# Kernel optimization log

Hardware: AMD Instinct MI355X
Metric: run time of the kernel (lower is better)

## Reference

```python
import jax, jax.numpy as jnp
import numpy as np

B_SZ, SEQ, D_MODEL = 64, 2048, 12
D_INNER, D_STATE, D_CONV, DT_RANK = 24, 16, 4, 4


def setup_inputs() -> dict:
    key = jax.random.key(0)
    ks = jax.random.split(key, 10)
    def n(k, shape, scale):
        return jax.random.normal(k, shape, jnp.float32) * scale
    return {
        "x": jax.random.normal(ks[0], (B_SZ, SEQ, D_MODEL), jnp.float32),
        "in_proj_w": n(ks[1], (2 * D_INNER, D_MODEL), 0.2),
        "conv_w": n(ks[2], (D_INNER, 1, D_CONV), 0.3),
        "conv_b": jnp.zeros((D_INNER,), jnp.float32),
        "x_proj_w": n(ks[3], (DT_RANK + 2 * D_STATE, D_INNER), 0.2),
        "dt_proj_w": n(ks[4], (D_INNER, DT_RANK), 0.5),
        "dt_proj_b": jax.random.uniform(ks[5], (D_INNER,), jnp.float32, -4.0, -2.0),
        "A_log": jnp.log(jnp.broadcast_to(jnp.arange(1, D_STATE + 1, dtype=jnp.float32), (D_INNER, D_STATE))),
        "D": jnp.ones((D_INNER,), jnp.float32),
        "out_proj_w": n(ks[6], (D_MODEL, D_INNER), 0.2),
        "fc_w": n(ks[7], (1, D_MODEL), 0.3),
        "fc_b": jnp.zeros((1,), jnp.float32),
    }


def _silu(v):
    return v * jax.nn.sigmoid(v)


def _mamba_head(x, in_proj_w, conv_w, conv_b, x_proj_w, dt_proj_w, dt_proj_b,
                A_log, D, out_proj_w, fc_w, fc_b):
    di = A_log.shape[0]
    ds = A_log.shape[1]
    dtr = dt_proj_w.shape[1]
    dc = conv_w.shape[-1]
    bsz = x.shape[0]

    # input projection -> [B,L,2*di], split into ssm branch and gate
    xz = jnp.einsum('bld,ed->ble', x, in_proj_w)
    x_in, z = jnp.split(xz, 2, axis=-1)

    # causal depthwise conv1d over time
    x_t = jnp.transpose(x_in, (0, 2, 1))                       # [B,di,L]
    x_t = jnp.pad(x_t, ((0, 0), (0, 0), (dc - 1, 0)))
    xc = jax.lax.conv_general_dilated(x_t, conv_w, (1,), 'VALID',
                                      feature_group_count=di)
    xc = _silu(jnp.transpose(xc + conv_b[None, :, None], (0, 2, 1)))  # [B,L,di]

    # data-dependent dt, B, C
    x_dbl = jnp.einsum('bld,ed->ble', xc, x_proj_w)
    dt, Bm, Cm = jnp.split(x_dbl, [dtr, dtr + ds], axis=-1)
    dt = jax.nn.softplus(jnp.einsum('blr,dr->bld', dt, dt_proj_w) + dt_proj_b)  # [B,L,di]

    A = -jnp.exp(A_log)                                        # [di,ds]
    dA = jnp.exp(dt[..., None] * A)                            # [B,L,di,ds]
    dBu = dt[..., None] * Bm[:, :, None, :] * xc[..., None]    # [B,L,di,ds]

    def step(h, inp):
        dA_t, dBu_t, C_t = inp
        h = dA_t * h + dBu_t                                   # [B,di,ds]
        y = jnp.einsum('bds,bs->bd', h, C_t)
        return h, y

    h0 = jnp.zeros((bsz, di, ds), x.dtype)
    _, ys = jax.lax.scan(step, h0, (jnp.swapaxes(dA, 0, 1),
                                    jnp.swapaxes(dBu, 0, 1),
                                    jnp.swapaxes(Cm, 0, 1)))
    y = jnp.swapaxes(ys, 0, 1) + xc * D                        # [B,L,di]
    y = y * _silu(z)
    out = jnp.einsum('bld,ed->ble', y, out_proj_w)             # [B,L,d_model]

    # final head on last timestep (SimpleMamba.linear)
    pred = out[:, -1, :] @ fc_w.T + fc_b                       # [B,1]
    return pred


def reference(x, in_proj_w, conv_w, conv_b, x_proj_w, dt_proj_w, dt_proj_b,
              A_log, D, out_proj_w, fc_w, fc_b):
    return _mamba_head(x, in_proj_w, conv_w, conv_b, x_proj_w, dt_proj_w,
                       dt_proj_b, A_log, D, out_proj_w, fc_w, fc_b)
```

## Files before the change

### kernel.cpp

```cpp
#include <hip/hip_runtime.h>
#include <math.h>

#define B_SZ 64
#define SEQ 2048
#define DM 12
#define DI 24
#define DS 16
#define DC 4
#define DTR 4
#define NSEG 32
#define SEGLEN 64
#define LP 68

__device__ __forceinline__ float silu_f(float v) { return v / (1.f + __expf(-v)); }
__device__ __forceinline__ float softplus_f(float v) {
    return fmaxf(v, 0.f) + __logf(1.f + __expf(-fabsf(v)));
}
__device__ __forceinline__ float dot12(const float4 w[3], float4 r0, float4 r1, float4 r2) {
    float s = 0.f;
    s = fmaf(w[0].x, r0.x, s); s = fmaf(w[0].y, r0.y, s);
    s = fmaf(w[0].z, r0.z, s); s = fmaf(w[0].w, r0.w, s);
    s = fmaf(w[1].x, r1.x, s); s = fmaf(w[1].y, r1.y, s);
    s = fmaf(w[1].z, r1.z, s); s = fmaf(w[1].w, r1.w, s);
    s = fmaf(w[2].x, r2.x, s); s = fmaf(w[2].y, r2.y, s);
    s = fmaf(w[2].z, r2.z, s); s = fmaf(w[2].w, r2.w, s);
    return s;
}

__global__ __launch_bounds__(384) void fused_scan_kernel(
    const float* __restrict__ x, const float* __restrict__ ipw,
    const float* __restrict__ cw, const float* __restrict__ cb,
    const float* __restrict__ xpw, const float* __restrict__ dpw,
    const float* __restrict__ dpb, const float* __restrict__ A_log,
    float* __restrict__ segA, float* __restrict__ segB)
{
    __shared__ __align__(16) float xc_s[DI][LP];
    __shared__ __align__(16) float dts[DI][LP];
    __shared__ __align__(16) float Bs[DS][LP];
    __shared__ __align__(16) float dtr_s[DTR][LP];

    const int tid = threadIdx.x;
    const int b = blockIdx.x >> 5, seg = blockIdx.x & 31;
    const int t0 = seg * SEGLEN;
    const int j = tid >> 6;
    const int t = tid & 63;
    const int d0 = j * 4;

    const float Aval = -__expf(A_log[tid]);

    float xc_loc[4];
    {
        float4 wA[4][3];
        float cwr[4][4];
        float acc[4];
#pragma unroll
        for (int i = 0; i < 4; ++i) {
            const float4* wp = (const float4*)(ipw + (d0 + i) * DM);
            wA[i][0] = wp[0]; wA[i][1] = wp[1]; wA[i][2] = wp[2];
            const float4 cw4 = *(const float4*)(cw + (d0 + i) * DC);
            cwr[i][0] = cw4.x; cwr[i][1] = cw4.y; cwr[i][2] = cw4.z; cwr[i][3] = cw4.w;
            acc[i] = cb[d0 + i];
        }
#pragma unroll
        for (int k = 0; k < DC; ++k) {
            int gt = t0 + t - (DC - 1) + k;
            float4 r0, r1, r2;
            if (gt >= 0) {
                const float4* xp = (const float4*)(x + ((size_t)b * SEQ + gt) * DM);
                r0 = xp[0]; r1 = xp[1]; r2 = xp[2];
            } else {
                r0 = make_float4(0.f, 0.f, 0.f, 0.f); r1 = r0; r2 = r0;
            }
#pragma unroll
            for (int i = 0; i < 4; ++i) {
                float xin = dot12(wA[i], r0, r1, r2);
                acc[i] = fmaf(xin, cwr[i][k], acc[i]);
            }
        }
#pragma unroll
        for (int i = 0; i < 4; ++i) {
            float v = silu_f(acc[i]);
            xc_loc[i] = v;
            xc_s[d0 + i][t] = v;
        }
    }
    __syncthreads();

    {
        float xc[DI];
#pragma unroll
        for (int d = 0; d < DI; ++d) xc[d] = xc_s[d][t];
        for (int r = j; r < DTR + DS; r += 6) {
            const float4* wr = (const float4*)(xpw + r * DI);
            float4 w4[6];
#pragma unroll
            for (int c = 0; c < 6; ++c) w4[c] = wr[c];
            float s = 0.f;
#pragma unroll
            for (int c = 0; c < 6; ++c) {
                s = fmaf(w4[c].x, xc[4 * c + 0], s);
                s = fmaf(w4[c].y, xc[4 * c + 1], s);
                s = fmaf(w4[c].z, xc[4 * c + 2], s);
                s = fmaf(w4[c].w, xc[4 * c + 3], s);
            }
            if (r < DTR) dtr_s[r][t] = s;
            else         Bs[r - DTR][t] = s;
        }
    }
    __syncthreads();

    {
        float dtr[DTR];
#pragma unroll
        for (int r = 0; r < DTR; ++r) dtr[r] = dtr_s[r][t];
#pragma unroll
        for (int i = 0; i < 4; ++i) {
            int d = d0 + i;
            const float4 w4 = *(const float4*)(dpw + d * DTR);
            float s = dpb[d];
            s = fmaf(dtr[0], w4.x, s); s = fmaf(dtr[1], w4.y, s);
            s = fmaf(dtr[2], w4.z, s); s = fmaf(dtr[3], w4.w, s);
            float dt = softplus_f(s);
            dts[d][t] = dt;
            xc_s[d][t] = dt * xc_loc[i];
        }
    }
    __syncthreads();

    {
        const int d = tid >> 4, s = tid & 15;
        float a_acc = 1.f, b_acc = 0.f;
        const float4* dtp = (const float4*)&dts[d][0];
        const float4* dup = (const float4*)&xc_s[d][0];
        const float4* Bp  = (const float4*)&Bs[s][0];
#pragma unroll 4
        for (int i = 0; i < SEGLEN / 4; ++i) {
            float4 dt4 = dtp[i], du4 = dup[i], B4 = Bp[i];
            float a;
            a = __expf(dt4.x * Aval); b_acc = fmaf(a, b_acc, du4.x * B4.x); a_acc *= a;
            a = __expf(dt4.y * Aval); b_acc = fmaf(a, b_acc, du4.y * B4.y); a_acc *= a;
            a = __expf(dt4.z * Aval); b_acc = fmaf(a, b_acc, du4.z * B4.z); a_acc *= a;
            a = __expf(dt4.w * Aval); b_acc = fmaf(a, b_acc, du4.w * B4.w); a_acc *= a;
        }
        size_t o = (size_t)blockIdx.x * (DI * DS) + tid;
        segA[o] = a_acc;
        segB[o] = b_acc;
    }
}

__global__ __launch_bounds__(384) void finish_kernel(
    const float* __restrict__ segA, const float* __restrict__ segB,
    const float* __restrict__ x, const float* __restrict__ ipw,
    const float* __restrict__ cw, const float* __restrict__ cb,
    const float* __restrict__ xpw, const float* __restrict__ Dv,
    const float* __restrict__ opw, const float* __restrict__ fcw,
    const float* __restrict__ fcb, float* __restrict__ out)
{
    int b = blockIdx.x, tid = threadIdx.x;

    float h = 0.f;
#pragma unroll
    for (int g = 0; g < NSEG; ++g) {
        size_t o = ((size_t)(b * NSEG + g)) * (DI * DS) + tid;
        h = fmaf(segA[o], h, segB[o]);
    }

    __shared__ float h_sh[DI * DS];
    __shared__ float xcl[DI], CL[DS], zv[DI], yv[DI], ov[DM];
    h_sh[tid] = h;

    const float* xr = x + ((size_t)b * SEQ + SEQ - 1) * DM;
    if (tid < DI) {
        float acc = cb[tid];
#pragma unroll
        for (int k = 0; k < DC; ++k) {
            const float* row = x + ((size_t)b * SEQ + (SEQ - DC + k)) * DM;
            float xin = 0.f;
#pragma unroll
            for (int m = 0; m < DM; ++m) xin = fmaf(row[m], ipw[tid * DM + m], xin);
            acc = fmaf(xin, cw[tid * DC + k], acc);
        }
        xcl[tid] = silu_f(acc);
        float s = 0.f;
#pragma unroll
        for (int m = 0; m < DM; ++m) s = fmaf(xr[m], ipw[(DI + tid) * DM + m], s);
        zv[tid] = s;
    }
    __syncthreads();

    if (tid < DS) {
        float s = 0.f;
#pragma unroll
        for (int d = 0; d < DI; ++d) s = fmaf(xcl[d], xpw[(DTR + DS + tid) * DI + d], s);
        CL[tid] = s;
    }
    __syncthreads();

    if (tid < DI) {
        float y = 0.f;
#pragma unroll
        for (int s2 = 0; s2 < DS; ++s2) y = fmaf(h_sh[tid * DS + s2], CL[s2], y);
        y = fmaf(xcl[tid], Dv[tid], y);
        yv[tid] = y * silu_f(zv[tid]);
    }
    __syncthreads();

    if (tid < DM) {
        float s = 0.f;
#pragma unroll
        for (int d = 0; d < DI; ++d) s = fmaf(yv[d], opw[tid * DI + d], s);
        ov[tid] = s;
    }
    __syncthreads();

    if (tid == 0) {
        float s = fcb[0];
#pragma unroll
        for (int e = 0; e < DM; ++e) s = fmaf(ov[e], fcw[e], s);
        out[b] = s;
    }
}

extern "C" void kernel_launch(void* const* d_in, const int* in_sizes, int n_in,
                              void* d_out, int out_size, void* d_ws, size_t ws_size,
                              hipStream_t stream)
{
    const float* x   = (const float*)d_in[0];
    const float* ipw = (const float*)d_in[1];
    const float* cw  = (const float*)d_in[2];
    const float* cb  = (const float*)d_in[3];
    const float* xpw = (const float*)d_in[4];
    const float* dpw = (const float*)d_in[5];
    const float* dpb = (const float*)d_in[6];
    const float* Al  = (const float*)d_in[7];
    const float* Dv  = (const float*)d_in[8];
    const float* opw = (const float*)d_in[9];
    const float* fcw = (const float*)d_in[10];
    const float* fcb = (const float*)d_in[11];

    float* segA = (float*)d_ws;
    float* segB = segA + (size_t)B_SZ * NSEG * DI * DS;

    fused_scan_kernel<<<B_SZ * NSEG, 384, 0, stream>>>(
        x, ipw, cw, cb, xpw, dpw, dpb, Al, segA, segB);
    finish_kernel<<<B_SZ, 384, 0, stream>>>(
        segA, segB, x, ipw, cw, cb, xpw, Dv, opw, fcw, fcb, (float*)d_out);
}
```

Measured before the change: 117.2 us.

## Fuse finish into scan kernel via last-block atomic counter; stage in_proj in LDS

```diff
diff --git a/kernel.cpp b/kernel.cpp
--- a/kernel.cpp
+++ b/kernel.cpp
@@ -27,17 +27,22 @@
     return s;
 }
 
-__global__ __launch_bounds__(384) void fused_scan_kernel(
+__global__ __launch_bounds__(384) void mamba_one_kernel(
     const float* __restrict__ x, const float* __restrict__ ipw,
     const float* __restrict__ cw, const float* __restrict__ cb,
     const float* __restrict__ xpw, const float* __restrict__ dpw,
     const float* __restrict__ dpb, const float* __restrict__ A_log,
-    float* __restrict__ segA, float* __restrict__ segB)
+    const float* __restrict__ Dv, const float* __restrict__ opw,
+    const float* __restrict__ fcw, const float* __restrict__ fcb,
+    float* __restrict__ segA, float* __restrict__ segB,
+    int* __restrict__ cnt, float* __restrict__ out)
 {
+    __shared__ __align__(16) float xin_s[DI][LP];
     __shared__ __align__(16) float xc_s[DI][LP];
     __shared__ __align__(16) float dts[DI][LP];
     __shared__ __align__(16) float Bs[DS][LP];
     __shared__ __align__(16) float dtr_s[DTR][LP];
+    __shared__ int is_last;
 
     const int tid = threadIdx.x;
     const int b = blockIdx.x >> 5, seg = blockIdx.x & 31;
@@ -48,38 +53,45 @@
 
     const float Aval = -__expf(A_log[tid]);
 
-    float xc_loc[4];
-    {
-        float4 wA[4][3];
-        float cwr[4][4];
-        float acc[4];
+    float4 wA[4][3];
+    float cwr[4][4], cbr[4];
+    {
 #pragma unroll
         for (int i = 0; i < 4; ++i) {
             const float4* wp = (const float4*)(ipw + (d0 + i) * DM);
             wA[i][0] = wp[0]; wA[i][1] = wp[1]; wA[i][2] = wp[2];
             const float4 cw4 = *(const float4*)(cw + (d0 + i) * DC);
             cwr[i][0] = cw4.x; cwr[i][1] = cw4.y; cwr[i][2] = cw4.z; cwr[i][3] = cw4.w;
-            acc[i] = cb[d0 + i];
-        }
-#pragma unroll
-        for (int k = 0; k < DC; ++k) {
-            int gt = t0 + t - (DC - 1) + k;
-            float4 r0, r1, r2;
+            cbr[i] = cb[d0 + i];
+        }
+        const float4* xp = (const float4*)(x + ((size_t)b * SEQ + (t0 + t)) * DM);
+        float4 r0 = xp[0], r1 = xp[1], r2 = xp[2];
+#pragma unroll
+        for (int i = 0; i < 4; ++i) xin_s[d0 + i][t + 3] = dot12(wA[i], r0, r1, r2);
+        if (t < 3) {
+            int gt = t0 + t - 3;
+            float4 h0, h1, h2;
             if (gt >= 0) {
-                const float4* xp = (const float4*)(x + ((size_t)b * SEQ + gt) * DM);
-                r0 = xp[0]; r1 = xp[1]; r2 = xp[2];
+                const float4* hp = (const float4*)(x + ((size_t)b * SEQ + gt) * DM);
+                h0 = hp[0]; h1 = hp[1]; h2 = hp[2];
             } else {
-                r0 = make_float4(0.f, 0.f, 0.f, 0.f); r1 = r0; r2 = r0;
+                h0 = make_float4(0.f, 0.f, 0.f, 0.f); h1 = h0; h2 = h0;
             }
 #pragma unroll
-            for (int i = 0; i < 4; ++i) {
-                float xin = dot12(wA[i], r0, r1, r2);
-                acc[i] = fmaf(xin, cwr[i][k], acc[i]);
-            }
-        }
+            for (int i = 0; i < 4; ++i) xin_s[d0 + i][t] = dot12(wA[i], h0, h1, h2);
+        }
+    }
+    __syncthreads();
+
+    float xc_loc[4];
+    {
 #pragma unroll
         for (int i = 0; i < 4; ++i) {
-            float v = silu_f(acc[i]);
+            float acc = cbr[i];
+#pragma unroll
+            for (int k = 0; k < DC; ++k)
+                acc = fmaf(cwr[i][k], xin_s[d0 + i][t + k], acc);
+            float v = silu_f(acc);
             xc_loc[i] = v;
             xc_s[d0 + i][t] = v;
         }
@@ -122,7 +134,7 @@
             s = fmaf(dtr[2], w4.z, s); s = fmaf(dtr[3], w4.w, s);
             float dt = softplus_f(s);
             dts[d][t] = dt;
-            xc_s[d][t] = dt * xc_loc[i];
+            xin_s[d][t] = dt * xc_loc[i];
         }
     }
     __syncthreads();
@@ -131,7 +143,7 @@
         const int d = tid >> 4, s = tid & 15;
         float a_acc = 1.f, b_acc = 0.f;
         const float4* dtp = (const float4*)&dts[d][0];
-        const float4* dup = (const float4*)&xc_s[d][0];
+        const float4* dup = (const float4*)&xin_s[d][0];
         const float4* Bp  = (const float4*)&Bs[s][0];
 #pragma unroll 4
         for (int i = 0; i < SEGLEN / 4; ++i) {
@@ -146,17 +158,19 @@
         segA[o] = a_acc;
         segB[o] = b_acc;
     }
-}
-
-__global__ __launch_bounds__(384) void finish_kernel(
-    const float* __restrict__ segA, const float* __restrict__ segB,
-    const float* __restrict__ x, const float* __restrict__ ipw,
-    const float* __restrict__ cw, const float* __restrict__ cb,
-    const float* __restrict__ xpw, const float* __restrict__ Dv,
-    const float* __restrict__ opw, const float* __restrict__ fcw,
-    const float* __restrict__ fcb, float* __restrict__ out)
-{
-    int b = blockIdx.x, tid = threadIdx.x;
+    __syncthreads();
+
+    if (tid == 0) {
+        __threadfence();
+        int old = atomicAdd(&cnt[b], 1);
+        is_last = (old == NSEG - 1);
+        if (is_last) __threadfence();
+    }
+    __syncthreads();
+    if (!is_last) return;
+
+    __shared__ float h_sh[DI * DS];
+    __shared__ float xcl[DI], CL[DS], zv[DI], yv[DI], ov[DM];
 
     float h = 0.f;
 #pragma unroll
@@ -164,9 +178,6 @@
         size_t o = ((size_t)(b * NSEG + g)) * (DI * DS) + tid;
         h = fmaf(segA[o], h, segB[o]);
     }
-
-    __shared__ float h_sh[DI * DS];
-    __shared__ float xcl[DI], CL[DS], zv[DI], yv[DI], ov[DM];
     h_sh[tid] = h;
 
     const float* xr = x + ((size_t)b * SEQ + SEQ - 1) * DM;
@@ -240,9 +251,10 @@
 
     float* segA = (float*)d_ws;
     float* segB = segA + (size_t)B_SZ * NSEG * DI * DS;
-
-    fused_scan_kernel<<<B_SZ * NSEG, 384, 0, stream>>>(
-        x, ipw, cw, cb, xpw, dpw, dpb, Al, segA, segB);
-    finish_kernel<<<B_SZ, 384, 0, stream>>>(
-        segA, segB, x, ipw, cw, cb, xpw, Dv, opw, fcw, fcb, (float*)d_out);
-}
+    int*   cnt  = (int*)(segB + (size_t)B_SZ * NSEG * DI * DS);
+
+    hipMemsetAsync(cnt, 0, B_SZ * sizeof(int), stream);
+    mamba_one_kernel<<<B_SZ * NSEG, 384, 0, stream>>>(
+        x, ipw, cw, cb, xpw, dpw, dpb, Al, Dv, opw, fcw, fcb,
+        segA, segB, cnt, (float*)d_out);
+}
```

Measured after the change: 159.2 us. +35.8%, slower.

## Restructure segment scan kernel into single-wave blocks with multi-chain per-thread scans

Applied to the files above, without the earlier changes.

```diff
diff --git a/kernel.cpp b/kernel.cpp
--- a/kernel.cpp
+++ b/kernel.cpp
@@ -16,135 +16,133 @@
 __device__ __forceinline__ float softplus_f(float v) {
     return fmaxf(v, 0.f) + __logf(1.f + __expf(-fabsf(v)));
 }
-__device__ __forceinline__ float dot12(const float4 w[3], float4 r0, float4 r1, float4 r2) {
+__device__ __forceinline__ float dot12w(float4 w0, float4 w1, float4 w2,
+                                        float4 r0, float4 r1, float4 r2) {
     float s = 0.f;
-    s = fmaf(w[0].x, r0.x, s); s = fmaf(w[0].y, r0.y, s);
-    s = fmaf(w[0].z, r0.z, s); s = fmaf(w[0].w, r0.w, s);
-    s = fmaf(w[1].x, r1.x, s); s = fmaf(w[1].y, r1.y, s);
-    s = fmaf(w[1].z, r1.z, s); s = fmaf(w[1].w, r1.w, s);
-    s = fmaf(w[2].x, r2.x, s); s = fmaf(w[2].y, r2.y, s);
-    s = fmaf(w[2].z, r2.z, s); s = fmaf(w[2].w, r2.w, s);
+    s = fmaf(w0.x, r0.x, s); s = fmaf(w0.y, r0.y, s);
+    s = fmaf(w0.z, r0.z, s); s = fmaf(w0.w, r0.w, s);
+    s = fmaf(w1.x, r1.x, s); s = fmaf(w1.y, r1.y, s);
+    s = fmaf(w1.z, r1.z, s); s = fmaf(w1.w, r1.w, s);
+    s = fmaf(w2.x, r2.x, s); s = fmaf(w2.y, r2.y, s);
+    s = fmaf(w2.z, r2.z, s); s = fmaf(w2.w, r2.w, s);
     return s;
 }
 
-__global__ __launch_bounds__(384) void fused_scan_kernel(
+__global__ __launch_bounds__(64) void fused_wave_kernel(
     const float* __restrict__ x, const float* __restrict__ ipw,
     const float* __restrict__ cw, const float* __restrict__ cb,
     const float* __restrict__ xpw, const float* __restrict__ dpw,
     const float* __restrict__ dpb, const float* __restrict__ A_log,
     float* __restrict__ segA, float* __restrict__ segB)
 {
-    __shared__ __align__(16) float xc_s[DI][LP];
-    __shared__ __align__(16) float dts[DI][LP];
-    __shared__ __align__(16) float Bs[DS][LP];
-    __shared__ __align__(16) float dtr_s[DTR][LP];
-
-    const int tid = threadIdx.x;
+    __shared__ __align__(16) float dts_s[DI][LP];
+    __shared__ __align__(16) float dus_s[DI][LP];
+    __shared__ __align__(16) float Bs_s[DS][LP];
+
+    const int lane = threadIdx.x;
     const int b = blockIdx.x >> 5, seg = blockIdx.x & 31;
     const int t0 = seg * SEGLEN;
-    const int j = tid >> 6;
-    const int t = tid & 63;
-    const int d0 = j * 4;
-
-    const float Aval = -__expf(A_log[tid]);
-
-    float xc_loc[4];
+    const int t = lane;
+
+#pragma unroll
+    for (int rep = 0; rep < 2; ++rep) {
+        int pp = lane + rep * 64;
+        if (pp < 3 * DI) {
+            int hr = pp / DI, d = pp % DI;
+            int row = t0 - 3 + hr;
+            float v = 0.f;
+            if (row >= 0) {
+                const float4* xp = (const float4*)(x + ((size_t)b * SEQ + row) * DM);
+                const float4* wp = (const float4*)(ipw + d * DM);
+                v = dot12w(wp[0], wp[1], wp[2], xp[0], xp[1], xp[2]);
+            }
+            dus_s[d][hr] = v;
+        }
+    }
+
     {
-        float4 wA[4][3];
-        float cwr[4][4];
-        float acc[4];
-#pragma unroll
-        for (int i = 0; i < 4; ++i) {
-            const float4* wp = (const float4*)(ipw + (d0 + i) * DM);
-            wA[i][0] = wp[0]; wA[i][1] = wp[1]; wA[i][2] = wp[2];
-            const float4 cw4 = *(const float4*)(cw + (d0 + i) * DC);
-            cwr[i][0] = cw4.x; cwr[i][1] = cw4.y; cwr[i][2] = cw4.z; cwr[i][3] = cw4.w;
-            acc[i] = cb[d0 + i];
-        }
-#pragma unroll
-        for (int k = 0; k < DC; ++k) {
-            int gt = t0 + t - (DC - 1) + k;
-            float4 r0, r1, r2;
-            if (gt >= 0) {
-                const float4* xp = (const float4*)(x + ((size_t)b * SEQ + gt) * DM);
-                r0 = xp[0]; r1 = xp[1]; r2 = xp[2];
-            } else {
-                r0 = make_float4(0.f, 0.f, 0.f, 0.f); r1 = r0; r2 = r0;
+        const float4* xp = (const float4*)(x + ((size_t)b * SEQ + (t0 + t)) * DM);
+        float4 r0 = xp[0], r1 = xp[1], r2 = xp[2];
+#pragma unroll
+        for (int d = 0; d < DI; ++d) {
+            const float4* wp = (const float4*)(ipw + d * DM);
+            dus_s[d][t + 3] = dot12w(wp[0], wp[1], wp[2], r0, r1, r2);
+        }
+    }
+    __syncthreads();
+
+    float xc[DI];
+#pragma unroll
+    for (int d = 0; d < DI; ++d) {
+        const float4 c4 = *(const float4*)(cw + d * DC);
+        float acc = cb[d];
+        acc = fmaf(c4.x, dus_s[d][t + 0], acc);
+        acc = fmaf(c4.y, dus_s[d][t + 1], acc);
+        acc = fmaf(c4.z, dus_s[d][t + 2], acc);
+        acc = fmaf(c4.w, dus_s[d][t + 3], acc);
+        xc[d] = silu_f(acc);
+    }
+    __syncthreads();
+
+    float dt_raw[DTR];
+#pragma unroll
+    for (int r = 0; r < DTR + DS; ++r) {
+        const float4* wr = (const float4*)(xpw + r * DI);
+        float s = 0.f;
+#pragma unroll
+        for (int c = 0; c < 6; ++c) {
+            float4 w4 = wr[c];
+            s = fmaf(w4.x, xc[4 * c + 0], s);
+            s = fmaf(w4.y, xc[4 * c + 1], s);
+            s = fmaf(w4.z, xc[4 * c + 2], s);
+            s = fmaf(w4.w, xc[4 * c + 3], s);
+        }
+        if (r < DTR) dt_raw[r] = s;
+        else         Bs_s[r - DTR][t] = s;
+    }
+
+#pragma unroll
+    for (int d = 0; d < DI; ++d) {
+        const float4 w4 = *(const float4*)(dpw + d * DTR);
+        float sv = dpb[d];
+        sv = fmaf(dt_raw[0], w4.x, sv); sv = fmaf(dt_raw[1], w4.y, sv);
+        sv = fmaf(dt_raw[2], w4.z, sv); sv = fmaf(dt_raw[3], w4.w, sv);
+        float dt = softplus_f(sv);
+        dts_s[d][t] = dt;
+        dus_s[d][t] = dt * xc[d];
+    }
+    __syncthreads();
+
+    {
+        const int s_ = lane & 15;
+        const int db = lane >> 4;
+        float Ap[6], aa[6], ba[6];
+#pragma unroll
+        for (int p = 0; p < 6; ++p) {
+            Ap[p] = -__expf(A_log[(4 * p + db) * DS + s_]);
+            aa[p] = 1.f; ba[p] = 0.f;
+        }
+#pragma unroll 2
+        for (int i = 0; i < SEGLEN / 4; ++i) {
+            const float4 B4 = *(const float4*)&Bs_s[s_][4 * i];
+#pragma unroll
+            for (int p = 0; p < 6; ++p) {
+                const int d = 4 * p + db;
+                const float4 dt4 = *(const float4*)&dts_s[d][4 * i];
+                const float4 du4 = *(const float4*)&dus_s[d][4 * i];
+                float a;
+                a = __expf(dt4.x * Ap[p]); ba[p] = fmaf(a, ba[p], du4.x * B4.x); aa[p] *= a;
+                a = __expf(dt4.y * Ap[p]); ba[p] = fmaf(a, ba[p], du4.y * B4.y); aa[p] *= a;
+                a = __expf(dt4.z * Ap[p]); ba[p] = fmaf(a, ba[p], du4.z * B4.z); aa[p] *= a;
+                a = __expf(dt4.w * Ap[p]); ba[p] = fmaf(a, ba[p], du4.w * B4.w); aa[p] *= a;
             }
-#pragma unroll
-            for (int i = 0; i < 4; ++i) {
-                float xin = dot12(wA[i], r0, r1, r2);
-                acc[i] = fmaf(xin, cwr[i][k], acc[i]);
-            }
-        }
-#pragma unroll
-        for (int i = 0; i < 4; ++i) {
-            float v = silu_f(acc[i]);
-            xc_loc[i] = v;
-            xc_s[d0 + i][t] = v;
-        }
-    }
-    __syncthreads();
-
-    {
-        float xc[DI];
-#pragma unroll
-        for (int d = 0; d < DI; ++d) xc[d] = xc_s[d][t];
-        for (int r = j; r < DTR + DS; r += 6) {
-            const float4* wr = (const float4*)(xpw + r * DI);
-            float4 w4[6];
-#pragma unroll
-            for (int c = 0; c < 6; ++c) w4[c] = wr[c];
-            float s = 0.f;
-#pragma unroll
-            for (int c = 0; c < 6; ++c) {
-                s = fmaf(w4[c].x, xc[4 * c + 0], s);
-                s = fmaf(w4[c].y, xc[4 * c + 1], s);
-                s = fmaf(w4[c].z, xc[4 * c + 2], s);
-                s = fmaf(w4[c].w, xc[4 * c + 3], s);
-            }
-            if (r < DTR) dtr_s[r][t] = s;
-            else         Bs[r - DTR][t] = s;
-        }
-    }
-    __syncthreads();
-
-    {
-        float dtr[DTR];
-#pragma unroll
-        for (int r = 0; r < DTR; ++r) dtr[r] = dtr_s[r][t];
-#pragma unroll
-        for (int i = 0; i < 4; ++i) {
-            int d = d0 + i;
-            const float4 w4 = *(const float4*)(dpw + d * DTR);
-            float s = dpb[d];
-            s = fmaf(dtr[0], w4.x, s); s = fmaf(dtr[1], w4.y, s);
-            s = fmaf(dtr[2], w4.z, s); s = fmaf(dtr[3], w4.w, s);
-            float dt = softplus_f(s);
-            dts[d][t] = dt;
-            xc_s[d][t] = dt * xc_loc[i];
-        }
-    }
-    __syncthreads();
-
-    {
-        const int d = tid >> 4, s = tid & 15;
-        float a_acc = 1.f, b_acc = 0.f;
-        const float4* dtp = (const float4*)&dts[d][0];
-        const float4* dup = (const float4*)&xc_s[d][0];
-        const float4* Bp  = (const float4*)&Bs[s][0];
-#pragma unroll 4
-        for (int i = 0; i < SEGLEN / 4; ++i) {
-            float4 dt4 = dtp[i], du4 = dup[i], B4 = Bp[i];
-            float a;
-            a = __expf(dt4.x * Aval); b_acc = fmaf(a, b_acc, du4.x * B4.x); a_acc *= a;
-            a = __expf(dt4.y * Aval); b_acc = fmaf(a, b_acc, du4.y * B4.y); a_acc *= a;
-            a = __expf(dt4.z * Aval); b_acc = fmaf(a, b_acc, du4.z * B4.z); a_acc *= a;
-            a = __expf(dt4.w * Aval); b_acc = fmaf(a, b_acc, du4.w * B4.w); a_acc *= a;
-        }
-        size_t o = (size_t)blockIdx.x * (DI * DS) + tid;
-        segA[o] = a_acc;
-        segB[o] = b_acc;
+        }
+        const size_t base = (size_t)blockIdx.x * (DI * DS);
+#pragma unroll
+        for (int p = 0; p < 6; ++p) {
+            segA[base + 64 * p + lane] = aa[p];
+            segB[base + 64 * p + lane] = ba[p];
+        }
     }
 }
 
@@ -241,7 +239,7 @@
     float* segA = (float*)d_ws;
     float* segB = segA + (size_t)B_SZ * NSEG * DI * DS;
 
-    fused_scan_kernel<<<B_SZ * NSEG, 384, 0, stream>>>(
+    fused_wave_kernel<<<B_SZ * NSEG, 64, 0, stream>>>(
         x, ipw, cw, cb, xpw, dpw, dpb, Al, segA, segB);
     finish_kernel<<<B_SZ, 384, 0, stream>>>(
         segA, segB, x, ipw, cw, cb, xpw, Dv, opw, fcw, fcb, (float*)d_out);
```

New measurement: 109.5 us. 1.07x faster.
